# Optimization experiments

Hardware: AMD Instinct MI355X
Metric: run time of the kernel (lower is better)

## Reference

```python
import jax, jax.numpy as jnp
import numpy as np

ALPHA = 0.2  # leaky_relu negative slope
NFEAT = 3    # node_feat_size for final tanh slice


def _init_linear(key, out_f, in_f):
    kw, kb = jax.random.split(key)
    scale = 1.0 / np.sqrt(in_f)
    w = jax.random.uniform(kw, (out_f, in_f), jnp.float32, -scale, scale)
    b = jax.random.uniform(kb, (out_f,), jnp.float32, -scale, scale)
    return w, b


def setup_inputs() -> dict:
    key = jax.random.key(0)
    ks = jax.random.split(key, 8)
    B, N, H = 64, 100, 32
    inp = {"x": jax.random.normal(ks[0], (B, N, H), jnp.float32)}
    # fe: [65 -> 96 -> 160 -> 192]; fn: [224 -> 256 -> 256 -> 32]
    fe_dims = [(96, 65), (160, 96), (192, 160)]
    fn_dims = [(256, 224), (256, 256), (32, 256)]
    for i, (o, f) in enumerate(fe_dims):
        w, b = _init_linear(ks[1 + i], o, f)
        inp[f"fe_w{i}"] = w
        inp[f"fe_b{i}"] = b
    for i, (o, f) in enumerate(fn_dims):
        w, b = _init_linear(ks[4 + i], o, f)
        inp[f"fn_w{i}"] = w
        inp[f"fn_b{i}"] = b
    return inp


def _forward(x, fe_params, fn_params):
    B, N, H = x.shape
    # --- getA: all-pairs edge features (pos_diffs) ---
    x1 = jnp.broadcast_to(x[:, :, None, :], (B, N, N, H))  # sender i
    x2 = jnp.broadcast_to(x[:, None, :, :], (B, N, N, H))  # receiver j
    dists = jnp.linalg.norm(x2[..., :2] - x1[..., :2] + 1e-12, axis=-1, keepdims=True)
    A = jnp.concatenate([x1, x2, dists], axis=-1)  # [B,N,N,2H+1]
    # --- edge MLP (all layers with leaky_relu) ---
    for w, b in fe_params:
        A = jax.nn.leaky_relu(jnp.einsum("bijf,of->bijo", A, w) + b, ALPHA)
    # sum-aggregate over neighbor axis j
    A = jnp.sum(A, axis=2)  # [B,N,fe_out]
    # --- node MLP (leaky_relu on all but last) ---
    h = jnp.concatenate([A, x], axis=-1)  # [B,N,fe_out+H]
    for w, b in fn_params[:-1]:
        h = jax.nn.leaky_relu(jnp.einsum("bnf,of->bno", h, w) + b, ALPHA)
    w, b = fn_params[-1]
    h = jnp.einsum("bnf,of->bno", h, w) + b  # [B,N,H]
    return jnp.tanh(h[..., :NFEAT])


def reference(x, fe_w0, fe_b0, fe_w1, fe_b1, fe_w2, fe_b2,
              fn_w0, fn_b0, fn_w1, fn_b1, fn_w2, fn_b2):
    fe_params = [(fe_w0, fe_b0), (fe_w1, fe_b1), (fe_w2, fe_b2)]
    fn_params = [(fn_w0, fn_b0), (fn_w1, fn_b1), (fn_w2, fn_b2)]
    return _forward(x, fe_params, fn_params)
```

## Files before the change

kernel.cpp:

```cpp
#include <hip/hip_runtime.h>
#include <math.h>

#define ALPHA 0.2f

typedef __attribute__((ext_vector_type(8))) short bf16x8;
typedef __attribute__((ext_vector_type(4))) float f32x4;

static __device__ __forceinline__ float lrelu(float v) {
    return fmaxf(v, ALPHA * v);
}
static __device__ __forceinline__ uint16_t f2b(float f) {
    union { float f; uint32_t u; } c; c.f = f;
    const uint32_t u = c.u + 0x7FFFu + ((c.u >> 16) & 1u);
    return (uint16_t)(u >> 16);
}
static __device__ __forceinline__ uint32_t cvt2(float lo, float hi) {
    uint32_t r;
    asm("v_cvt_pk_bf16_f32 %0, %1, %2" : "=v"(r) : "v"(lo), "v"(hi));
    return r;
}

__global__ __launch_bounds__(256) void precompute(
    const float* __restrict__ x, const float* __restrict__ w0,
    const float* __restrict__ b0, const float* __restrict__ w1,
    const float* __restrict__ w2, const float* __restrict__ f0,
    const float* __restrict__ f1,
    float* __restrict__ base0T, float* __restrict__ Gp,
    float* __restrict__ xyt, float* __restrict__ wd0,
    uint16_t* __restrict__ wb1, uint16_t* __restrict__ wb2,
    uint16_t* __restrict__ wfn0, uint16_t* __restrict__ wfn1,
    float* __restrict__ hin)
{
    const int blk = blockIdx.x, t = threadIdx.x;
    if (blk >= 256) {
        const int t0 = (blk - 256) * 256 + t;
        for (int i = t0; i < 160 * 96;  i += 7168) wb1[i]  = f2b(w1[i]);
        for (int i = t0; i < 192 * 160; i += 7168) wb2[i]  = f2b(w2[i]);
        for (int i = t0; i < 256 * 224; i += 7168) wfn0[i] = f2b(f0[i]);
        for (int i = t0; i < 256 * 256; i += 7168) wfn1[i] = f2b(f1[i]);
        if (t0 < 96) wd0[t0] = w0[t0 * 65 + 64];
        return;
    }
    __shared__ float W0s[96 * 65];
    __shared__ float xs[25 * 32];
    const int r0 = blk * 25;
    for (int i = t; i < 96 * 65; i += 256) W0s[i] = w0[i];
    for (int i = t; i < 800; i += 256) xs[i] = x[r0 * 32 + i];
    __syncthreads();
    for (int it = 0; it < 19; ++it) {
        const int q = t + 256 * it;
        if (q < 4800) {
            const int row = q / 192, oi = q - row * 192;
            const int o = (oi < 96) ? oi : oi - 96;
            const float* wr = W0s + o * 65 + ((oi < 96) ? 0 : 32);
            const float* xr = xs + row * 32;
            float a = (oi < 96) ? b0[o] : 0.0f;
#pragma unroll
            for (int k = 0; k < 32; ++k) a += wr[k] * xr[k];
            if (oi < 96) base0T[(r0 + row) * 96 + o] = a;
            else         Gp[(o >> 3) * 51200 + (r0 + row) * 8 + (o & 7)] = a;
        }
    }
    for (int i = t; i < 50; i += 256)
        xyt[(r0 + (i >> 1)) * 2 + (i & 1)] = xs[(i >> 1) * 32 + (i & 1)];
    for (int i = t; i < 800; i += 256)
        hin[(r0 + (i >> 5)) * 256 + 192 + (i & 31)] = xs[i];
}

__global__ __launch_bounds__(512, 4) void edge_kernel(
    const float* __restrict__ base0T, const float* __restrict__ Gp,
    const float* __restrict__ xyt, const float* __restrict__ wd0,
    const float* __restrict__ b1f, const float* __restrict__ b2f,
    const uint16_t* __restrict__ wb1, const uint16_t* __restrict__ wb2,
    float* __restrict__ hin)
{
    __shared__ __align__(16) uint16_t H1[112 * 104];
    __shared__ __align__(16) uint16_t H2[112 * 168];

    const int bi = blockIdx.x, b = bi / 100;
    const int t = threadIdx.x, lane = t & 63, w = t >> 6;
    const int col = lane & 15, g = lane >> 4;

    if (t < 448) {
        const int row = t >> 2, c = t & 3;
        if (row < 100) {
            const int jg = b * 100 + row;
            const float2 pj = *(const float2*)(xyt + 2 * jg);
            const float2 pi = *(const float2*)(xyt + 2 * bi);
            const float dx = pj.x - pi.x + 1e-12f, dy = pj.y - pi.y + 1e-12f;
            const float d = sqrtf(dx * dx + dy * dy);
#pragma unroll
            for (int i = 0; i < 3; ++i) {
                const int c8 = c * 3 + i, ow = c8 * 8;
                const float* gp = Gp + c8 * 51200 + jg * 8;
                const f32x4 g0 = *(const f32x4*)(gp);
                const f32x4 g1 = *(const f32x4*)(gp + 4);
                const f32x4 c0 = *(const f32x4*)(base0T + bi * 96 + ow);
                const f32x4 c1 = *(const f32x4*)(base0T + bi * 96 + ow + 4);
                const f32x4 w0v = *(const f32x4*)(wd0 + ow);
                const f32x4 w1v = *(const f32x4*)(wd0 + ow + 4);
                float v[8];
#pragma unroll
                for (int e = 0; e < 4; ++e) {
                    v[e]     = lrelu(g0[e] + c0[e] + w0v[e] * d);
                    v[4 + e] = lrelu(g1[e] + c1[e] + w1v[e] * d);
                }
                *(uint4*)(H1 + row * 104 + ow) =
                    (uint4){cvt2(v[0], v[1]), cvt2(v[2], v[3]),
                            cvt2(v[4], v[5]), cvt2(v[6], v[7])};
            }
        } else {
            const uint4 z = {0u, 0u, 0u, 0u};
#pragma unroll
            for (int i = 0; i < 3; ++i)
                *(uint4*)(H1 + row * 104 + (c * 3 + i) * 8) = z;
        }
    }
    __syncthreads();

    if (w < 5) {
        const int nt0 = 2 * w, nt1 = 2 * w + 1;
        f32x4 acc0[7], acc1[7];
        const f32x4 bb0 = *(const f32x4*)(b1f + nt0 * 16 + 4 * g);
        const f32x4 bb1 = *(const f32x4*)(b1f + nt1 * 16 + 4 * g);
#pragma unroll
        for (int m = 0; m < 7; ++m) { acc0[m] = bb0; acc1[m] = bb1; }
        __builtin_amdgcn_s_setprio(1);
#pragma unroll
        for (int kt = 0; kt < 3; ++kt) {
            const bf16x8 wf0 = *(const bf16x8*)(wb1 + (nt0 * 16 + col) * 96 + kt * 32 + 8 * g);
            const bf16x8 wf1 = *(const bf16x8*)(wb1 + (nt1 * 16 + col) * 96 + kt * 32 + 8 * g);
#pragma unroll
            for (int m = 0; m < 7; ++m) {
                const bf16x8 hf = *(const bf16x8*)(H1 + (m * 16 + col) * 104 + kt * 32 + 8 * g);
                acc0[m] = __builtin_amdgcn_mfma_f32_16x16x32_bf16(wf0, hf, acc0[m], 0, 0, 0);
                acc1[m] = __builtin_amdgcn_mfma_f32_16x16x32_bf16(wf1, hf, acc1[m], 0, 0, 0);
            }
        }
        __builtin_amdgcn_s_setprio(0);
#pragma unroll
        for (int m = 0; m < 7; ++m) {
            {
                const uint32_t p01 = cvt2(lrelu(acc0[m][0]), lrelu(acc0[m][1]));
                const uint32_t p23 = cvt2(lrelu(acc0[m][2]), lrelu(acc0[m][3]));
                *(uint2*)(H2 + (m * 16 + col) * 168 + nt0 * 16 + 4 * g) = (uint2){p01, p23};
            }
            {
                const uint32_t p01 = cvt2(lrelu(acc1[m][0]), lrelu(acc1[m][1]));
                const uint32_t p23 = cvt2(lrelu(acc1[m][2]), lrelu(acc1[m][3]));
                *(uint2*)(H2 + (m * 16 + col) * 168 + nt1 * 16 + 4 * g) = (uint2){p01, p23};
            }
        }
    }
    __syncthreads();

    if (w < 6) {
        const int nt0 = 2 * w, nt1 = 2 * w + 1;
        f32x4 acc0[7], acc1[7];
        const float bv0 = b2f[nt0 * 16 + col];
        const float bv1 = b2f[nt1 * 16 + col];
#pragma unroll
        for (int m = 0; m < 7; ++m) {
            acc0[m] = (f32x4){bv0, bv0, bv0, bv0};
            acc1[m] = (f32x4){bv1, bv1, bv1, bv1};
        }
        __builtin_amdgcn_s_setprio(1);
#pragma unroll
        for (int kt = 0; kt < 5; ++kt) {
            const bf16x8 bf0 = *(const bf16x8*)(wb2 + (nt0 * 16 + col) * 160 + kt * 32 + 8 * g);
            const bf16x8 bf1 = *(const bf16x8*)(wb2 + (nt1 * 16 + col) * 160 + kt * 32 + 8 * g);
#pragma unroll
            for (int m = 0; m < 7; ++m) {
                const bf16x8 af = *(const bf16x8*)(H2 + (m * 16 + col) * 168 + kt * 32 + 8 * g);
                acc0[m] = __builtin_amdgcn_mfma_f32_16x16x32_bf16(af, bf0, acc0[m], 0, 0, 0);
                acc1[m] = __builtin_amdgcn_mfma_f32_16x16x32_bf16(af, bf1, acc1[m], 0, 0, 0);
            }
        }
        __builtin_amdgcn_s_setprio(0);
        float s0 = 0.0f, s1 = 0.0f;
#pragma unroll
        for (int m = 0; m < 7; ++m) {
            const int rowbase = m * 16 + 4 * g;
#pragma unroll
            for (int r = 0; r < 4; ++r) {
                const bool ok = (m < 6) || (rowbase + r < 100);
                if (ok) {
                    s0 += lrelu(acc0[m][r]);
                    s1 += lrelu(acc1[m][r]);
                }
            }
        }
        s0 += __shfl_xor(s0, 16);
        s0 += __shfl_xor(s0, 32);
        s1 += __shfl_xor(s1, 16);
        s1 += __shfl_xor(s1, 32);
        if (lane < 16) {
            hin[bi * 256 + nt0 * 16 + col] = s0;
            hin[bi * 256 + nt1 * 16 + col] = s1;
        }
    }
}

__global__ __launch_bounds__(256) void node_kernel(
    const float* __restrict__ hin,
    const uint16_t* __restrict__ wfn0, const float* __restrict__ fb0,
    const uint16_t* __restrict__ wfn1, const float* __restrict__ fb1,
    const float* __restrict__ fw2, const float* __restrict__ fb2,
    float* __restrict__ out)
{
    __shared__ __align__(16) uint16_t RA[16 * 264];
    __shared__ __align__(16) uint16_t RH[16 * 264];
    const int t = threadIdx.x, lane = t & 63, wave = t >> 6;
    const int col = lane & 15, g = lane >> 4;
    const int r0 = blockIdx.x * 16;

    for (int r = wave; r < 16; r += 4) {
        const float* src = hin + (r0 + r) * 256;
        for (int c = lane; c < 224; c += 64)
            RA[r * 232 + c] = f2b(src[c]);
    }
    __syncthreads();
    {
        f32x4 acc[4];
#pragma unroll
        for (int s = 0; s < 4; ++s) {
            const float bv = fb0[(wave + 4 * s) * 16 + col];
            acc[s] = (f32x4){bv, bv, bv, bv};
        }
#pragma unroll
        for (int kt = 0; kt < 7; ++kt) {
            const bf16x8 afr = *(const bf16x8*)(RA + col * 232 + kt * 32 + 8 * g);
#pragma unroll
            for (int s = 0; s < 4; ++s) {
                const bf16x8 bfr = *(const bf16x8*)(
                    wfn0 + ((wave + 4 * s) * 16 + col) * 224 + kt * 32 + 8 * g);
                acc[s] = __builtin_amdgcn_mfma_f32_16x16x32_bf16(afr, bfr, acc[s], 0, 0, 0);
            }
        }
#pragma unroll
        for (int s = 0; s < 4; ++s)
#pragma unroll
            for (int r = 0; r < 4; ++r)
                RH[(4 * g + r) * 264 + (wave + 4 * s) * 16 + col] = f2b(lrelu(acc[s][r]));
    }
    __syncthreads();
    {
        f32x4 acc[4];
#pragma unroll
        for (int s = 0; s < 4; ++s) {
            const float bv = fb1[(wave + 4 * s) * 16 + col];
            acc[s] = (f32x4){bv, bv, bv, bv};
        }
#pragma unroll
        for (int kt = 0; kt < 8; ++kt) {
            const bf16x8 afr = *(const bf16x8*)(RH + col * 264 + kt * 32 + 8 * g);
#pragma unroll
            for (int s = 0; s < 4; ++s) {
                const bf16x8 bfr = *(const bf16x8*)(
                    wfn1 + ((wave + 4 * s) * 16 + col) * 256 + kt * 32 + 8 * g);
                acc[s] = __builtin_amdgcn_mfma_f32_16x16x32_bf16(afr, bfr, acc[s], 0, 0, 0);
            }
        }
        __syncthreads();
#pragma unroll
        for (int s = 0; s < 4; ++s)
#pragma unroll
            for (int r = 0; r < 4; ++r)
                RA[(4 * g + r) * 264 + (wave + 4 * s) * 16 + col] = f2b(lrelu(acc[s][r]));
    }
    __syncthreads();
    const int row = t >> 4, u = t & 15;
    float h = 0.0f;
    if (u < 12) {
        const int o = u >> 2, ks = u & 3;
        const float* wv = fw2 + o * 256 + ks * 64;
        const uint16_t* hr = RA + row * 264 + ks * 64;
        float a = 0.0f;
#pragma unroll 8
        for (int k = 0; k < 64; k += 4) {
            const ushort4 hv = *(const ushort4*)(hr + k);
            union { uint32_t u; float f; } c0, c1, c2, c3;
            c0.u = (uint32_t)hv.x << 16; c1.u = (uint32_t)hv.y << 16;
            c2.u = (uint32_t)hv.z << 16; c3.u = (uint32_t)hv.w << 16;
            a += wv[k] * c0.f + wv[k + 1] * c1.f + wv[k + 2] * c2.f + wv[k + 3] * c3.f;
        }
        h = a;
    }
    h += __shfl_xor(h, 1);
    h += __shfl_xor(h, 2);
    if (u < 12 && (u & 3) == 0)
        out[(r0 + row) * 3 + (u >> 2)] = tanhf(h + fb2[u >> 2]);
}

extern "C" void kernel_launch(void* const* d_in, const int* in_sizes, int n_in,
                              void* d_out, int out_size, void* d_ws, size_t ws_size,
                              hipStream_t stream) {
    (void)in_sizes; (void)n_in; (void)out_size; (void)ws_size;
    const float* x     = (const float*)d_in[0];
    const float* fe_w0 = (const float*)d_in[1];
    const float* fe_b0 = (const float*)d_in[2];
    const float* fe_w1 = (const float*)d_in[3];
    const float* fe_b1 = (const float*)d_in[4];
    const float* fe_w2 = (const float*)d_in[5];
    const float* fe_b2 = (const float*)d_in[6];
    const float* fn_w0 = (const float*)d_in[7];
    const float* fn_b0 = (const float*)d_in[8];
    const float* fn_w1 = (const float*)d_in[9];
    const float* fn_b1 = (const float*)d_in[10];
    const float* fn_w2 = (const float*)d_in[11];
    const float* fn_b2 = (const float*)d_in[12];
    float* out = (float*)d_out;

    float* buf0   = (float*)d_ws;
    float* base0T = buf0 + (size_t)6400 * 256;
    float* Gp     = base0T + 6400 * 96;
    float* xyt    = Gp + 6400 * 96;
    float* wd0    = xyt + 12800;
    uint16_t* wb1  = (uint16_t*)(wd0 + 128);
    uint16_t* wb2  = wb1 + 160 * 96;
    uint16_t* wfn0 = wb2 + 192 * 160;
    uint16_t* wfn1 = wfn0 + 256 * 224;

    precompute<<<284, 256, 0, stream>>>(x, fe_w0, fe_b0, fe_w1, fe_w2,
                                        fn_w0, fn_w1,
                                        base0T, Gp, xyt, wd0,
                                        wb1, wb2, wfn0, wfn1, buf0);
    edge_kernel<<<6400, 512, 0, stream>>>(base0T, Gp, xyt, wd0,
                                          fe_b1, fe_b2, wb1, wb2, buf0);
    node_kernel<<<400, 256, 0, stream>>>(buf0, wfn0, fn_b0, wfn1, fn_b1,
                                         fn_w2, fn_b2, out);
}
```

Measured before the change: 153.1 us.

## Split edge MLP layers 1-2 into two row chunks to shrink H2 and accumulators

The layer-1 and layer-2 MFMA stages of the edge kernel now run in two sub-passes over row tiles (4 then 3), so the H2 staging buffer holds only 64 rows and each wave keeps 4 instead of 7 accumulator pairs. Padding rows are handled by zeroing the bias for padded entries rather than masking the final sum. The aim is lower LDS and register use, allowing more resident blocks per CU. In exchange it adds an extra barrier, reloads the weight fragments for each sub-pass, and the bias-zeroing trick depends on padded H1 rows being zero.

```diff
diff --git a/kernel.cpp b/kernel.cpp
--- a/kernel.cpp
+++ b/kernel.cpp
@@ -75,7 +75,7 @@
     float* __restrict__ hin)
 {
     __shared__ __align__(16) uint16_t H1[112 * 104];
-    __shared__ __align__(16) uint16_t H2[112 * 168];
+    __shared__ __align__(16) uint16_t H2[64 * 168];
 
     const int bi = blockIdx.x, b = bi / 100;
     const int t = threadIdx.x, lane = t & 63, w = t >> 6;
@@ -118,78 +118,92 @@
     }
     __syncthreads();
 
-    if (w < 5) {
-        const int nt0 = 2 * w, nt1 = 2 * w + 1;
-        f32x4 acc0[7], acc1[7];
-        const f32x4 bb0 = *(const f32x4*)(b1f + nt0 * 16 + 4 * g);
-        const f32x4 bb1 = *(const f32x4*)(b1f + nt1 * 16 + 4 * g);
-#pragma unroll
-        for (int m = 0; m < 7; ++m) { acc0[m] = bb0; acc1[m] = bb1; }
-        __builtin_amdgcn_s_setprio(1);
-#pragma unroll
-        for (int kt = 0; kt < 3; ++kt) {
-            const bf16x8 wf0 = *(const bf16x8*)(wb1 + (nt0 * 16 + col) * 96 + kt * 32 + 8 * g);
-            const bf16x8 wf1 = *(const bf16x8*)(wb1 + (nt1 * 16 + col) * 96 + kt * 32 + 8 * g);
-#pragma unroll
-            for (int m = 0; m < 7; ++m) {
-                const bf16x8 hf = *(const bf16x8*)(H1 + (m * 16 + col) * 104 + kt * 32 + 8 * g);
-                acc0[m] = __builtin_amdgcn_mfma_f32_16x16x32_bf16(wf0, hf, acc0[m], 0, 0, 0);
-                acc1[m] = __builtin_amdgcn_mfma_f32_16x16x32_bf16(wf1, hf, acc1[m], 0, 0, 0);
-            }
-        }
-        __builtin_amdgcn_s_setprio(0);
-#pragma unroll
-        for (int m = 0; m < 7; ++m) {
-            {
-                const uint32_t p01 = cvt2(lrelu(acc0[m][0]), lrelu(acc0[m][1]));
-                const uint32_t p23 = cvt2(lrelu(acc0[m][2]), lrelu(acc0[m][3]));
-                *(uint2*)(H2 + (m * 16 + col) * 168 + nt0 * 16 + 4 * g) = (uint2){p01, p23};
-            }
-            {
-                const uint32_t p01 = cvt2(lrelu(acc1[m][0]), lrelu(acc1[m][1]));
-                const uint32_t p23 = cvt2(lrelu(acc1[m][2]), lrelu(acc1[m][3]));
-                *(uint2*)(H2 + (m * 16 + col) * 168 + nt1 * 16 + 4 * g) = (uint2){p01, p23};
-            }
-        }
-    }
-    __syncthreads();
-
-    if (w < 6) {
-        const int nt0 = 2 * w, nt1 = 2 * w + 1;
-        f32x4 acc0[7], acc1[7];
-        const float bv0 = b2f[nt0 * 16 + col];
-        const float bv1 = b2f[nt1 * 16 + col];
-#pragma unroll
-        for (int m = 0; m < 7; ++m) {
-            acc0[m] = (f32x4){bv0, bv0, bv0, bv0};
-            acc1[m] = (f32x4){bv1, bv1, bv1, bv1};
-        }
-        __builtin_amdgcn_s_setprio(1);
-#pragma unroll
-        for (int kt = 0; kt < 5; ++kt) {
-            const bf16x8 bf0 = *(const bf16x8*)(wb2 + (nt0 * 16 + col) * 160 + kt * 32 + 8 * g);
-            const bf16x8 bf1 = *(const bf16x8*)(wb2 + (nt1 * 16 + col) * 160 + kt * 32 + 8 * g);
-#pragma unroll
-            for (int m = 0; m < 7; ++m) {
-                const bf16x8 af = *(const bf16x8*)(H2 + (m * 16 + col) * 168 + kt * 32 + 8 * g);
-                acc0[m] = __builtin_amdgcn_mfma_f32_16x16x32_bf16(af, bf0, acc0[m], 0, 0, 0);
-                acc1[m] = __builtin_amdgcn_mfma_f32_16x16x32_bf16(af, bf1, acc1[m], 0, 0, 0);
-            }
-        }
-        __builtin_amdgcn_s_setprio(0);
-        float s0 = 0.0f, s1 = 0.0f;
-#pragma unroll
-        for (int m = 0; m < 7; ++m) {
-            const int rowbase = m * 16 + 4 * g;
-#pragma unroll
-            for (int r = 0; r < 4; ++r) {
-                const bool ok = (m < 6) || (rowbase + r < 100);
-                if (ok) {
+    float s0 = 0.0f, s1 = 0.0f;
+    const int nt0 = 2 * w, nt1 = 2 * w + 1;
+
+#pragma unroll
+    for (int sub = 0; sub < 2; ++sub) {
+        const int MT = sub ? 3 : 4;
+        const int mb = sub ? 4 : 0;
+
+        if (w < 5) {
+            f32x4 acc0[4], acc1[4];
+            const f32x4 bb0 = *(const f32x4*)(b1f + nt0 * 16 + 4 * g);
+            const f32x4 bb1 = *(const f32x4*)(b1f + nt1 * 16 + 4 * g);
+            const f32x4 zz = {0.f, 0.f, 0.f, 0.f};
+#pragma unroll
+            for (int m = 0; m < 4; ++m) if (m < MT) {
+                const bool pad = (sub == 1 && m == 2 && col >= 4);
+                acc0[m] = pad ? zz : bb0;
+                acc1[m] = pad ? zz : bb1;
+            }
+            __builtin_amdgcn_s_setprio(1);
+#pragma unroll
+            for (int kt = 0; kt < 3; ++kt) {
+                const bf16x8 wf0 = *(const bf16x8*)(wb1 + (nt0 * 16 + col) * 96 + kt * 32 + 8 * g);
+                const bf16x8 wf1 = *(const bf16x8*)(wb1 + (nt1 * 16 + col) * 96 + kt * 32 + 8 * g);
+#pragma unroll
+                for (int m = 0; m < 4; ++m) if (m < MT) {
+                    const bf16x8 hf = *(const bf16x8*)(H1 + ((mb + m) * 16 + col) * 104 + kt * 32 + 8 * g);
+                    acc0[m] = __builtin_amdgcn_mfma_f32_16x16x32_bf16(wf0, hf, acc0[m], 0, 0, 0);
+                    acc1[m] = __builtin_amdgcn_mfma_f32_16x16x32_bf16(wf1, hf, acc1[m], 0, 0, 0);
+                }
+            }
+            __builtin_amdgcn_s_setprio(0);
+#pragma unroll
+            for (int m = 0; m < 4; ++m) if (m < MT) {
+                {
+                    const uint32_t p01 = cvt2(lrelu(acc0[m][0]), lrelu(acc0[m][1]));
+                    const uint32_t p23 = cvt2(lrelu(acc0[m][2]), lrelu(acc0[m][3]));
+                    *(uint2*)(H2 + (m * 16 + col) * 168 + nt0 * 16 + 4 * g) = (uint2){p01, p23};
+                }
+                {
+                    const uint32_t p01 = cvt2(lrelu(acc1[m][0]), lrelu(acc1[m][1]));
+                    const uint32_t p23 = cvt2(lrelu(acc1[m][2]), lrelu(acc1[m][3]));
+                    *(uint2*)(H2 + (m * 16 + col) * 168 + nt1 * 16 + 4 * g) = (uint2){p01, p23};
+                }
+            }
+        }
+        __syncthreads();
+
+        if (w < 6) {
+            f32x4 acc0[4], acc1[4];
+            const float bv0 = b2f[nt0 * 16 + col];
+            const float bv1 = b2f[nt1 * 16 + col];
+#pragma unroll
+            for (int m = 0; m < 4; ++m) if (m < MT) {
+                const bool pad = (sub == 1 && m == 2 && g != 0);
+                const float a0 = pad ? 0.0f : bv0;
+                const float a1 = pad ? 0.0f : bv1;
+                acc0[m] = (f32x4){a0, a0, a0, a0};
+                acc1[m] = (f32x4){a1, a1, a1, a1};
+            }
+            __builtin_amdgcn_s_setprio(1);
+#pragma unroll
+            for (int kt = 0; kt < 5; ++kt) {
+                const bf16x8 bf0 = *(const bf16x8*)(wb2 + (nt0 * 16 + col) * 160 + kt * 32 + 8 * g);
+                const bf16x8 bf1 = *(const bf16x8*)(wb2 + (nt1 * 16 + col) * 160 + kt * 32 + 8 * g);
+#pragma unroll
+                for (int m = 0; m < 4; ++m) if (m < MT) {
+                    const bf16x8 af = *(const bf16x8*)(H2 + (m * 16 + col) * 168 + kt * 32 + 8 * g);
+                    acc0[m] = __builtin_amdgcn_mfma_f32_16x16x32_bf16(af, bf0, acc0[m], 0, 0, 0);
+                    acc1[m] = __builtin_amdgcn_mfma_f32_16x16x32_bf16(af, bf1, acc1[m], 0, 0, 0);
+                }
+            }
+            __builtin_amdgcn_s_setprio(0);
+#pragma unroll
+            for (int m = 0; m < 4; ++m) if (m < MT) {
+#pragma unroll
+                for (int r = 0; r < 4; ++r) {
                     s0 += lrelu(acc0[m][r]);
                     s1 += lrelu(acc1[m][r]);
                 }
             }
         }
+        if (sub == 0) __syncthreads();
+    }
+
+    if (w < 6) {
         s0 += __shfl_xor(s0, 16);
         s0 += __shfl_xor(s0, 32);
         s1 += __shfl_xor(s1, 16);
```

Result: slower. 164.5 us (+7.4%).
